# Optimization experiments

Hardware: AMD Instinct MI355X
Metric: run time of the kernel (lower is better)

Reference implementation:

```python
import jax, jax.numpy as jnp
import numpy as np

DIM = 1024
N_HEADS = 16
HEAD_DIM = DIM // N_HEADS


def setup_inputs() -> dict:
    key = jax.random.key(0)
    ks = jax.random.split(key, 5)
    B, L = 2, 2048
    q = jax.random.normal(ks[0], (B, L, DIM), dtype=jnp.float32)
    # nn.Linear weights: shape [out_features, in_features], applied as x @ W.T
    scale = 1.0 / np.sqrt(DIM)
    Wq = jax.random.normal(ks[1], (DIM, DIM), dtype=jnp.float32) * scale
    Wk = jax.random.normal(ks[2], (DIM, DIM), dtype=jnp.float32) * scale
    Wv = jax.random.normal(ks[3], (DIM, DIM), dtype=jnp.float32) * scale
    Wo = jax.random.normal(ks[4], (DIM, DIM), dtype=jnp.float32) * scale
    return {"q": q, "Wq": Wq, "Wk": Wk, "Wv": Wv, "Wo": Wo}


def reference(q, Wq, Wk, Wv, Wo):
    B, L, _ = q.shape
    kv = q  # self-attention (kv=None path)
    # projections: x @ W.T, then split heads: b l (h d) -> b h l d
    def split_heads(x):
        return x.reshape(B, L, N_HEADS, HEAD_DIM).transpose(0, 2, 1, 3)
    qh = split_heads(q @ Wq.T)
    kh = split_heads(kv @ Wk.T)
    vh = split_heads(kv @ Wv.T)
    # scaled dot-product attention; scale = sqrt(head_dim)
    scores = jnp.einsum('bhid,bhjd->bhij', qh, kh) / jnp.sqrt(
        jnp.asarray(HEAD_DIM, dtype=qh.dtype))
    attn = jax.nn.softmax(scores, axis=-1)
    out = jnp.einsum('bhij,bhjd->bhid', attn, vh)
    # b h l d -> b l (h d)
    out = out.transpose(0, 2, 1, 3).reshape(B, L, DIM)
    return out @ Wo.T
```

## Files before the change

### kernel.cpp

```cpp
#include <hip/hip_runtime.h>


#define DIMN 1024
#define NH 16
#define HD 64
#define BB 2
#define LL 2048

typedef float f32x4 __attribute__((ext_vector_type(4)));
typedef short s16x8 __attribute__((ext_vector_type(8)));

#define QSCALE 0.18033688011112042f

static __device__ __forceinline__ unsigned short f2bf(float f) {
  unsigned u = __float_as_uint(f);
  u += 0x7fffu + ((u >> 16) & 1u);
  return (unsigned short)(u >> 16);
}
static __device__ __forceinline__ unsigned packbf2(float lo, float hi) {
  return (unsigned)f2bf(lo) | ((unsigned)f2bf(hi) << 16);
}
static __device__ __forceinline__ float xexp2(float x) {
#if __has_builtin(__builtin_amdgcn_exp2f)
  return __builtin_amdgcn_exp2f(x);
#else
  return exp2f(x);
#endif
}
static __device__ __forceinline__ s16x8 cvt8(float4 a, float4 b) {
  s16x8 r;
  r[0] = (short)f2bf(a.x); r[1] = (short)f2bf(a.y);
  r[2] = (short)f2bf(a.z); r[3] = (short)f2bf(a.w);
  r[4] = (short)f2bf(b.x); r[5] = (short)f2bf(b.y);
  r[6] = (short)f2bf(b.z); r[7] = (short)f2bf(b.w);
  return r;
}
static __device__ __forceinline__ void gld16(const unsigned short* g,
                                             unsigned short* l) {
#if __has_builtin(__builtin_amdgcn_global_load_lds)
  __builtin_amdgcn_global_load_lds(
      (const __attribute__((address_space(1))) void*)g,
      (__attribute__((address_space(3))) void*)l, 16, 0, 0);
#else
  ((uint4*)l)[threadIdx.x & 63] = ((const uint4*)g)[0];
#endif
}

static __device__ __forceinline__ int vpos(int s128) {
  return (s128 & 0x60) | ((s128 & 0x0C) << 1) | ((s128 & 0x10) >> 2) | (s128 & 3);
}

__global__ __launch_bounds__(256) void cvt_all(
    const float* __restrict__ X, const float* __restrict__ Wq,
    const float* __restrict__ Wk, const float* __restrict__ Wv,
    const float* __restrict__ Wo, unsigned short* __restrict__ out) {
  const int blk = blockIdx.x;
  const float* src;
  unsigned short* dst;
  size_t off;
  if (blk < 2048) {
    src = X; dst = out; off = (size_t)blk * 2048;
  } else {
    int s = (blk - 2048) >> 9;
    src = (s == 0) ? Wq : (s == 1) ? Wk : (s == 2) ? Wv : Wo;
    dst = out + ((size_t)1 << 22) + (size_t)s * (1u << 20);
    off = (size_t)((blk - 2048) & 511) * 2048;
  }
  size_t i = off + (size_t)threadIdx.x * 8;
  float4 v0 = *(const float4*)(src + i);
  float4 v1 = *(const float4*)(src + i + 4);
  uint4 o;
  o.x = packbf2(v0.x, v0.y); o.y = packbf2(v0.z, v0.w);
  o.z = packbf2(v1.x, v1.y); o.w = packbf2(v1.z, v1.w);
  *(uint4*)(dst + i) = o;
}

__global__ __launch_bounds__(256) void gemm_qkv(
    const unsigned short* __restrict__ Xb, const unsigned short* __restrict__ Wb,
    unsigned short* __restrict__ Qb, unsigned short* __restrict__ Kb,
    unsigned short* __restrict__ VT) {
  __shared__ __align__(16) unsigned short Al[128 * 64];
  __shared__ __align__(16) unsigned short Bl[128 * 64];
  const int lin = blockIdx.x;
  const int xcd = lin & 7, sblk = lin >> 3;
  const int m0 = ((xcd & 3) * 8 + (sblk & 7)) * 128;
  const int n0g = ((xcd >> 2) * 12 + (sblk >> 3)) * 128;
  const int sel = n0g >> 10;
  const int tid = threadIdx.x;
  const int w = tid >> 6, lane = tid & 63;
  const int c = lane & 15, quad = lane >> 4;
  const int wm = (w & 1) * 64, wn = (w >> 1) * 64;

  f32x4 zero = {0.f, 0.f, 0.f, 0.f};
  f32x4 acc[4][4];
#pragma unroll
  for (int i = 0; i < 4; ++i)
#pragma unroll
    for (int j = 0; j < 4; ++j) acc[i][j] = zero;

  const int l8 = lane >> 3, p8 = lane & 7;
  const unsigned short* gA = Xb + (size_t)(m0 + w * 8 + l8) * DIMN + ((p8 ^ l8) * 8);
  const unsigned short* gB = Wb + (size_t)(n0g + w * 8 + l8) * DIMN + ((p8 ^ l8) * 8);
  unsigned short* lA = Al + (w * 8) * 64;
  unsigned short* lB = Bl + (w * 8) * 64;
  const int c7 = c & 7;

  for (int k0 = 0; k0 < DIMN; k0 += 64) {
    __syncthreads();
#pragma unroll
    for (int r = 0; r < 4; ++r) {
      gld16(gA + k0 + (size_t)(r * 32) * DIMN, lA + r * 32 * 64);
      gld16(gB + k0 + (size_t)(r * 32) * DIMN, lB + r * 32 * 64);
    }
    __syncthreads();
#pragma unroll
    for (int f = 0; f < 2; ++f) {
      const int rd = ((f * 4 + quad) ^ c7) * 8;
      s16x8 a[4], b[4];
#pragma unroll
      for (int i = 0; i < 4; ++i)
        a[i] = *(const s16x8*)&Al[(wm + i * 16 + c) * 64 + rd];
#pragma unroll
      for (int j = 0; j < 4; ++j)
        b[j] = *(const s16x8*)&Bl[(wn + j * 16 + c) * 64 + rd];
      if (sel != 2) {
#pragma unroll
        for (int i = 0; i < 4; ++i)
#pragma unroll
          for (int j = 0; j < 4; ++j)
            acc[i][j] = __builtin_amdgcn_mfma_f32_16x16x32_bf16(b[j], a[i], acc[i][j], 0, 0, 0);
      } else {
#pragma unroll
        for (int i = 0; i < 4; ++i)
#pragma unroll
          for (int j = 0; j < 4; ++j)
            acc[i][j] = __builtin_amdgcn_mfma_f32_16x16x32_bf16(a[i], b[j], acc[i][j], 0, 0, 0);
      }
    }
  }

  const int n0 = n0g & 1023;
  if (sel != 2) {
    unsigned short* Out = (sel == 0) ? Qb : Kb;
    const float scale = (sel == 0) ? QSCALE : 1.0f;
    const int bi = (m0 + wm) >> 11;
#pragma unroll
    for (int i = 0; i < 4; ++i) {
      const int li = (m0 + wm + i * 16 + c) & 2047;
#pragma unroll
      for (int j = 0; j < 4; ++j) {
        const int nq = n0 + wn + j * 16 + quad * 4;
        const int h = nq >> 6, d = nq & 63;
        uint2 st;
        st.x = packbf2(acc[i][j][0] * scale, acc[i][j][1] * scale);
        st.y = packbf2(acc[i][j][2] * scale, acc[i][j][3] * scale);
        *(uint2*)&Out[(((size_t)bi * NH + h) * LL + li) * HD + d] = st;
      }
    }
  } else {
    const int bi = m0 >> 11;
    const int mlo = m0 & 2047;
#pragma unroll
    for (int i = 0; i < 4; ++i) {
      const int pos = mlo + vpos(wm + i * 16 + quad * 4);
#pragma unroll
      for (int j = 0; j < 4; ++j) {
        const int nv = n0 + wn + j * 16 + c;
        const int h = nv >> 6, d = nv & 63;
        uint2 st;
        st.x = packbf2(acc[i][j][0], acc[i][j][1]);
        st.y = packbf2(acc[i][j][2], acc[i][j][3]);
        *(uint2*)&VT[(((size_t)bi * NH + h) * HD + d) * LL + pos] = st;
      }
    }
  }
}

__global__ __launch_bounds__(256) void gemm_o(
    const unsigned short* __restrict__ A, const unsigned short* __restrict__ Wob,
    float* __restrict__ Out) {
  __shared__ __align__(16) unsigned short Al[128 * 64];
  __shared__ __align__(16) unsigned short Bl[64 * 64];
  const int lin = blockIdx.x;
  const int xcd = lin & 7, sblk = lin >> 3;
  const int m0 = ((sblk >> 4) * 8 + xcd) * 128;
  const int n0 = (sblk & 15) * 64;
  const int tid = threadIdx.x;
  const int w = tid >> 6, lane = tid & 63;
  const int c = lane & 15, quad = lane >> 4;
  const int wm = (w & 1) * 64, wn = (w >> 1) * 32;

  f32x4 zero = {0.f, 0.f, 0.f, 0.f};
  f32x4 acc[4][2];
#pragma unroll
  for (int i = 0; i < 4; ++i)
#pragma unroll
    for (int j = 0; j < 2; ++j) acc[i][j] = zero;

  const int l8 = lane >> 3, p8 = lane & 7;
  const unsigned short* gA = A + (size_t)(m0 + w * 8 + l8) * DIMN + ((p8 ^ l8) * 8);
  const unsigned short* gB = Wob + (size_t)(n0 + w * 8 + l8) * DIMN + ((p8 ^ l8) * 8);
  unsigned short* lA = Al + (w * 8) * 64;
  unsigned short* lB = Bl + (w * 8) * 64;
  const int c7 = c & 7;

  for (int k0 = 0; k0 < DIMN; k0 += 64) {
    __syncthreads();
#pragma unroll
    for (int r = 0; r < 4; ++r)
      gld16(gA + k0 + (size_t)(r * 32) * DIMN, lA + r * 32 * 64);
#pragma unroll
    for (int r = 0; r < 2; ++r)
      gld16(gB + k0 + (size_t)(r * 32) * DIMN, lB + r * 32 * 64);
    __syncthreads();
#pragma unroll
    for (int f = 0; f < 2; ++f) {
      const int rd = ((f * 4 + quad) ^ c7) * 8;
      s16x8 a[4], b[2];
#pragma unroll
      for (int i = 0; i < 4; ++i)
        a[i] = *(const s16x8*)&Al[(wm + i * 16 + c) * 64 + rd];
#pragma unroll
      for (int j = 0; j < 2; ++j)
        b[j] = *(const s16x8*)&Bl[(wn + j * 16 + c) * 64 + rd];
#pragma unroll
      for (int i = 0; i < 4; ++i)
#pragma unroll
        for (int j = 0; j < 2; ++j)
          acc[i][j] = __builtin_amdgcn_mfma_f32_16x16x32_bf16(a[i], b[j], acc[i][j], 0, 0, 0);
    }
  }

#pragma unroll
  for (int i = 0; i < 4; ++i)
#pragma unroll
    for (int j = 0; j < 2; ++j)
#pragma unroll
      for (int r = 0; r < 4; ++r)
        Out[(size_t)(m0 + wm + i * 16 + quad * 4 + r) * DIMN + n0 + wn + j * 16 + c] =
            acc[i][j][r];
}

__global__ __launch_bounds__(256, 2) void attn7(
    const unsigned short* __restrict__ Qb, const unsigned short* __restrict__ Kb,
    const unsigned short* __restrict__ VT, unsigned short* __restrict__ AO) {
  __shared__ __align__(16) unsigned short Kl[2 * 128 * 64];
  __shared__ __align__(16) unsigned short Vtl[2 * 64 * 128];

  const int lin = blockIdx.x;
  const int xcd = lin & 7, sblk = lin >> 3;
  const int bh = (sblk >> 4) * 8 + xcd;
  const int qi = sblk & 15;
  const int tid = threadIdx.x;
  const int w = tid >> 6, lane = tid & 63;
  const int c = lane & 15, quad = lane >> 4;
  const int qa = qi * 128 + w * 16;
  const int qbr = qa + 64;

  const unsigned short* Qh = Qb + (size_t)bh * LL * HD;
  const unsigned short* Kh = Kb + (size_t)bh * LL * HD;
  const unsigned short* Vh = VT + (size_t)bh * HD * LL;

  s16x8 qA0 = *(const s16x8*)(Qh + (size_t)(qa + c) * HD + quad * 8);
  s16x8 qA1 = *(const s16x8*)(Qh + (size_t)(qa + c) * HD + 32 + quad * 8);
  s16x8 qB0 = *(const s16x8*)(Qh + (size_t)(qbr + c) * HD + quad * 8);
  s16x8 qB1 = *(const s16x8*)(Qh + (size_t)(qbr + c) * HD + 32 + quad * 8);

  f32x4 zero = {0.f, 0.f, 0.f, 0.f};
  f32x4 oA[4], oB[4];
  float lsumA = 0.f, lsumB = 0.f;
#pragma unroll
  for (int dc = 0; dc < 4; ++dc) { oA[dc] = zero; oB[dc] = zero; }

  const int l8 = lane >> 3, p8 = lane & 7;
  const unsigned short* gK = Kh + (size_t)(w * 32 + l8) * HD + ((p8 ^ l8) * 8);
  const int l16 = lane >> 4, p16 = lane & 15;
  const int vr0 = w * 16 + l16;
  const int vr1 = w * 16 + 4 + l16;
  const int vr2 = w * 16 + 8 + l16;
  const int vr3 = w * 16 + 12 + l16;
  const unsigned short* gV0 = Vh + (size_t)vr0 * LL + ((p16 ^ (vr0 & 15)) * 8);
  const unsigned short* gV1 = Vh + (size_t)vr1 * LL + ((p16 ^ (vr1 & 15)) * 8);
  const unsigned short* gV2 = Vh + (size_t)vr2 * LL + ((p16 ^ (vr2 & 15)) * 8);
  const unsigned short* gV3 = Vh + (size_t)vr3 * LL + ((p16 ^ (vr3 & 15)) * 8);

  const int kpa = (quad ^ (c & 7)) * 8;
  const int kpb = ((quad + 4) ^ (c & 7)) * 8;

#define STAGE(buf, k0)                                                        \
  do {                                                                        \
    unsigned short* lK_ = Kl + (buf) * (128 * 64) + (w * 32) * 64;            \
    unsigned short* lV_ = Vtl + (buf) * (64 * 128) + (w * 16) * 128;          \
    gld16(gK + (size_t)(k0) * HD, lK_);                                       \
    gld16(gK + (size_t)((k0) + 8) * HD, lK_ + 8 * 64);                        \
    gld16(gK + (size_t)((k0) + 16) * HD, lK_ + 16 * 64);                      \
    gld16(gK + (size_t)((k0) + 24) * HD, lK_ + 24 * 64);                      \
    gld16(gV0 + (k0), lV_);                                                   \
    gld16(gV1 + (k0), lV_ + 4 * 128);                                         \
    gld16(gV2 + (k0), lV_ + 8 * 128);                                         \
    gld16(gV3 + (k0), lV_ + 12 * 128);                                        \
  } while (0)

  STAGE(0, 0);

  for (int it = 0; it < LL / 128; ++it) {
    __syncthreads();
    if (it + 1 < LL / 128) STAGE((it + 1) & 1, (it + 1) * 128);
    const unsigned short* Kt = Kl + (it & 1) * (128 * 64);
    const unsigned short* Vt = Vtl + (it & 1) * (64 * 128);

#pragma unroll
    for (int g = 0; g < 2; ++g) {
      f32x4 sA[4], sB[4];
#pragma unroll
      for (int t4 = 0; t4 < 4; ++t4) {
        const unsigned short* kr = Kt + ((g * 4 + t4) * 16 + c) * 64;
        s16x8 kfa = *(const s16x8*)(kr + kpa);
        s16x8 kfb = *(const s16x8*)(kr + kpb);
        sA[t4] = __builtin_amdgcn_mfma_f32_16x16x32_bf16(kfa, qA0, zero, 0, 0, 0);
        sA[t4] = __builtin_amdgcn_mfma_f32_16x16x32_bf16(kfb, qA1, sA[t4], 0, 0, 0);
        sB[t4] = __builtin_amdgcn_mfma_f32_16x16x32_bf16(kfa, qB0, zero, 0, 0, 0);
        sB[t4] = __builtin_amdgcn_mfma_f32_16x16x32_bf16(kfb, qB1, sB[t4], 0, 0, 0);
      }
      float pA[4][4], pB[4][4];
      float accA = 0.f, accB = 0.f;
#pragma unroll
      for (int t4 = 0; t4 < 4; ++t4)
#pragma unroll
        for (int r = 0; r < 4; ++r) {
          float eA = xexp2(sA[t4][r]);
          float eB = xexp2(sB[t4][r]);
          pA[t4][r] = eA; accA += eA;
          pB[t4][r] = eB; accB += eB;
        }
      lsumA += accA;
      lsumB += accB;
#pragma unroll
      for (int kh = 0; kh < 2; ++kh) {
        const int kk = g * 2 + kh;
        unsigned puA[4], puB[4];
        puA[0] = __builtin_amdgcn_perm(__float_as_uint(pA[2 * kh][1]),
                                       __float_as_uint(pA[2 * kh][0]), 0x07060302u);
        puA[1] = __builtin_amdgcn_perm(__float_as_uint(pA[2 * kh][3]),
                                       __float_as_uint(pA[2 * kh][2]), 0x07060302u);
        puA[2] = __builtin_amdgcn_perm(__float_as_uint(pA[2 * kh + 1][1]),
                                       __float_as_uint(pA[2 * kh + 1][0]), 0x07060302u);
        puA[3] = __builtin_amdgcn_perm(__float_as_uint(pA[2 * kh + 1][3]),
                                       __float_as_uint(pA[2 * kh + 1][2]), 0x07060302u);
        puB[0] = __builtin_amdgcn_perm(__float_as_uint(pB[2 * kh][1]),
                                       __float_as_uint(pB[2 * kh][0]), 0x07060302u);
        puB[1] = __builtin_amdgcn_perm(__float_as_uint(pB[2 * kh][3]),
                                       __float_as_uint(pB[2 * kh][2]), 0x07060302u);
        puB[2] = __builtin_amdgcn_perm(__float_as_uint(pB[2 * kh + 1][1]),
                                       __float_as_uint(pB[2 * kh + 1][0]), 0x07060302u);
        puB[3] = __builtin_amdgcn_perm(__float_as_uint(pB[2 * kh + 1][3]),
                                       __float_as_uint(pB[2 * kh + 1][2]), 0x07060302u);
        s16x8 pfA = *(const s16x8*)puA;
        s16x8 pfB = *(const s16x8*)puB;
#pragma unroll
        for (int dc = 0; dc < 4; ++dc) {
          s16x8 vf = *(const s16x8*)(Vt + (dc * 16 + c) * 128 + (((kk * 4 + quad) ^ c) * 8));
          oA[dc] = __builtin_amdgcn_mfma_f32_16x16x32_bf16(vf, pfA, oA[dc], 0, 0, 0);
          oB[dc] = __builtin_amdgcn_mfma_f32_16x16x32_bf16(vf, pfB, oB[dc], 0, 0, 0);
        }
      }
    }
  }
#undef STAGE

  const int bi = bh >> 4, h = bh & 15;
  float lA = lsumA;
  lA += __shfl_xor(lA, 16);
  lA += __shfl_xor(lA, 32);
  float invA = 1.0f / lA;
  float lB = lsumB;
  lB += __shfl_xor(lB, 16);
  lB += __shfl_xor(lB, 32);
  float invB = 1.0f / lB;
  unsigned short* dstA = AO + ((size_t)bi * LL + qa + c) * DIMN + h * HD + quad * 4;
  unsigned short* dstB = AO + ((size_t)bi * LL + qbr + c) * DIMN + h * HD + quad * 4;
#pragma unroll
  for (int dc = 0; dc < 4; ++dc) {
    uint2 stA, stB;
    stA.x = packbf2(oA[dc][0] * invA, oA[dc][1] * invA);
    stA.y = packbf2(oA[dc][2] * invA, oA[dc][3] * invA);
    stB.x = packbf2(oB[dc][0] * invB, oB[dc][1] * invB);
    stB.y = packbf2(oB[dc][2] * invB, oB[dc][3] * invB);
    *(uint2*)(dstA + dc * 16) = stA;
    *(uint2*)(dstB + dc * 16) = stB;
  }
}

__global__ __launch_bounds__(64) void qkv_proj_f(
    const float* __restrict__ X, const float* __restrict__ Wq,
    const float* __restrict__ Wk, const float* __restrict__ Wv,
    unsigned short* __restrict__ Qb, unsigned short* __restrict__ Kb,
    unsigned short* __restrict__ VT) {
  const int m0 = blockIdx.x * 64;
  const int n0g = blockIdx.y * 64;
  const int sel = n0g >> 10;
  const int n0 = n0g & 1023;
  const float* W = (sel == 0) ? Wq : (sel == 1) ? Wk : Wv;
  const int lane = threadIdx.x;
  const int c = lane & 15, quad = lane >> 4;

  f32x4 zero = {0.f, 0.f, 0.f, 0.f};
  f32x4 acc[4][4];
#pragma unroll
  for (int i = 0; i < 4; ++i)
#pragma unroll
    for (int j = 0; j < 4; ++j) acc[i][j] = zero;

  const float* ab = X + (size_t)(m0 + c) * DIMN + quad * 8;
  const float* bb = W + (size_t)(n0 + c) * DIMN + quad * 8;

  for (int k0 = 0; k0 < DIMN; k0 += 32) {
    s16x8 a[4], b[4];
#pragma unroll
    for (int i = 0; i < 4; ++i) {
      const float* pp = ab + i * 16 * DIMN + k0;
      a[i] = cvt8(*(const float4*)pp, *(const float4*)(pp + 4));
    }
#pragma unroll
    for (int j = 0; j < 4; ++j) {
      const float* pp = bb + j * 16 * DIMN + k0;
      b[j] = cvt8(*(const float4*)pp, *(const float4*)(pp + 4));
    }
    if (sel != 2) {
#pragma unroll
      for (int i = 0; i < 4; ++i)
#pragma unroll
        for (int j = 0; j < 4; ++j)
          acc[i][j] = __builtin_amdgcn_mfma_f32_16x16x32_bf16(a[i], b[j], acc[i][j], 0, 0, 0);
    } else {
#pragma unroll
      for (int i = 0; i < 4; ++i)
#pragma unroll
        for (int j = 0; j < 4; ++j)
          acc[i][j] = __builtin_amdgcn_mfma_f32_16x16x32_bf16(b[j], a[i], acc[i][j], 0, 0, 0);
    }
  }

  if (sel != 2) {
    unsigned short* Out = (sel == 0) ? Qb : Kb;
    const float scale = (sel == 0) ? QSCALE : 1.0f;
#pragma unroll
    for (int i = 0; i < 4; ++i)
#pragma unroll
      for (int j = 0; j < 4; ++j)
#pragma unroll
        for (int r = 0; r < 4; ++r) {
          int row = m0 + i * 16 + quad * 4 + r;
          int nl = n0 + j * 16 + c;
          int bi = row >> 11, li = row & 2047;
          int h = nl >> 6, d = nl & 63;
          Out[(((size_t)bi * NH + h) * LL + li) * HD + d] = f2bf(acc[i][j][r] * scale);
        }
  } else {
#pragma unroll
    for (int i = 0; i < 4; ++i) {
#pragma unroll
      for (int j = 0; j < 4; ++j)
#pragma unroll
        for (int r = 0; r < 4; ++r) {
          int n = n0 + j * 16 + quad * 4 + r;
          int s128 = (m0 & 64) + i * 16 + c;
          int m = (m0 & ~127) + vpos(s128);
          int h = n >> 6, d = n & 63;
          int bi = m0 >> 11;
          VT[(((size_t)bi * NH + h) * HD + d) * LL + (m & 2047)] = f2bf(acc[i][j][r]);
        }
    }
  }
}

__global__ __launch_bounds__(64) void o_proj_f(
    const unsigned short* __restrict__ A, const float* __restrict__ Wo,
    float* __restrict__ Out) {
  const int m0 = blockIdx.x * 64, n0 = blockIdx.y * 64;
  const int lane = threadIdx.x;
  const int c = lane & 15, quad = lane >> 4;

  f32x4 zero = {0.f, 0.f, 0.f, 0.f};
  f32x4 acc[4][4];
#pragma unroll
  for (int i = 0; i < 4; ++i)
#pragma unroll
    for (int j = 0; j < 4; ++j) acc[i][j] = zero;

  const unsigned short* ab = A + (size_t)(m0 + c) * DIMN + quad * 8;
  const float* bb = Wo + (size_t)(n0 + c) * DIMN + quad * 8;

  for (int k0 = 0; k0 < DIMN; k0 += 32) {
    s16x8 a[4], b[4];
#pragma unroll
    for (int i = 0; i < 4; ++i) a[i] = *(const s16x8*)(ab + i * 16 * DIMN + k0);
#pragma unroll
    for (int j = 0; j < 4; ++j) {
      const float* pp = bb + j * 16 * DIMN + k0;
      b[j] = cvt8(*(const float4*)pp, *(const float4*)(pp + 4));
    }
#pragma unroll
    for (int i = 0; i < 4; ++i)
#pragma unroll
      for (int j = 0; j < 4; ++j)
        acc[i][j] = __builtin_amdgcn_mfma_f32_16x16x32_bf16(a[i], b[j], acc[i][j], 0, 0, 0);
  }

#pragma unroll
  for (int i = 0; i < 4; ++i)
#pragma unroll
    for (int j = 0; j < 4; ++j)
#pragma unroll
      for (int r = 0; r < 4; ++r)
        Out[(size_t)(m0 + i * 16 + quad * 4 + r) * DIMN + n0 + j * 16 + c] = acc[i][j][r];
}

extern "C" void kernel_launch(void* const* d_in, const int* in_sizes, int n_in,
                              void* d_out, int out_size, void* d_ws, size_t ws_size,
                              hipStream_t stream) {
  const float* X = (const float*)d_in[0];
  const float* Wq = (const float*)d_in[1];
  const float* Wk = (const float*)d_in[2];
  const float* Wv = (const float*)d_in[3];
  const float* Wo = (const float*)d_in[4];
  float* Out = (float*)d_out;

  const size_t M1 = (size_t)1 << 20;
  unsigned short* ws16 = (unsigned short*)d_ws;

  if (ws_size >= (size_t)48 * 1024 * 1024) {
    unsigned short* Xb = ws16;
    unsigned short* Wb = ws16 + 4 * M1;
    unsigned short* Qb = ws16 + 8 * M1;
    unsigned short* Kb = ws16 + 12 * M1;
    unsigned short* VT = ws16 + 16 * M1;
    unsigned short* AO = ws16 + 20 * M1;
    cvt_all<<<4096, 256, 0, stream>>>(X, Wq, Wk, Wv, Wo, ws16);
    gemm_qkv<<<768, 256, 0, stream>>>(Xb, Wb, Qb, Kb, VT);
    attn7<<<512, 256, 0, stream>>>(Qb, Kb, VT, AO);
    gemm_o<<<512, 256, 0, stream>>>(AO, Wb + 3 * M1, Out);
  } else {
    unsigned short* Qb = ws16;
    unsigned short* Kb = ws16 + 4 * M1;
    unsigned short* VT = ws16 + 8 * M1;
    unsigned short* AO = ws16 + 12 * M1;
    qkv_proj_f<<<dim3(64, 48), 64, 0, stream>>>(X, Wq, Wk, Wv, Qb, Kb, VT);
    attn7<<<512, 256, 0, stream>>>(Qb, Kb, VT, AO);
    o_proj_f<<<dim3(64, 16), 64, 0, stream>>>(AO, Wo, Out);
  }
}
```

Baseline: 174.2 us.

## Software-pipeline attention: overlap QK^T of next tile with PV of current

Restructures the attention main loop so QK^T and softmax for K tile it+1 run in the same iteration as the PV product for V tile it. This puts the exp/perm VALU work between MFMA bursts so the two can overlap. K and V staging are split so K is prefetched two tiles ahead and V one tile ahead. s_setprio raises wave priority around the MFMA phases. The cost is more live registers (probabilities for a whole tile are held across phases), which may cause spills at 2 waves per SIMD.

```diff
diff --git a/kernel.cpp b/kernel.cpp
--- a/kernel.cpp
+++ b/kernel.cpp
@@ -241,7 +241,7 @@
             acc[i][j][r];
 }
 
-__global__ __launch_bounds__(256, 2) void attn7(
+__global__ __launch_bounds__(256, 2) void attn8(
     const unsigned short* __restrict__ Qb, const unsigned short* __restrict__ Kb,
     const unsigned short* __restrict__ VT, unsigned short* __restrict__ AO) {
   __shared__ __align__(16) unsigned short Kl[2 * 128 * 64];
@@ -287,86 +287,137 @@
   const int kpa = (quad ^ (c & 7)) * 8;
   const int kpb = ((quad + 4) ^ (c & 7)) * 8;
 
-#define STAGE(buf, k0)                                                        \
+#define STAGE_K(buf, k0)                                                      \
   do {                                                                        \
     unsigned short* lK_ = Kl + (buf) * (128 * 64) + (w * 32) * 64;            \
-    unsigned short* lV_ = Vtl + (buf) * (64 * 128) + (w * 16) * 128;          \
     gld16(gK + (size_t)(k0) * HD, lK_);                                       \
     gld16(gK + (size_t)((k0) + 8) * HD, lK_ + 8 * 64);                        \
     gld16(gK + (size_t)((k0) + 16) * HD, lK_ + 16 * 64);                      \
     gld16(gK + (size_t)((k0) + 24) * HD, lK_ + 24 * 64);                      \
+  } while (0)
+#define STAGE_V(buf, k0)                                                      \
+  do {                                                                        \
+    unsigned short* lV_ = Vtl + (buf) * (64 * 128) + (w * 16) * 128;          \
     gld16(gV0 + (k0), lV_);                                                   \
     gld16(gV1 + (k0), lV_ + 4 * 128);                                         \
     gld16(gV2 + (k0), lV_ + 8 * 128);                                         \
     gld16(gV3 + (k0), lV_ + 12 * 128);                                        \
   } while (0)
 
-  STAGE(0, 0);
-
-  for (int it = 0; it < LL / 128; ++it) {
+#define QK_PHASE(Kt, g)                                                       \
+  do {                                                                        \
+    _Pragma("unroll")                                                         \
+    for (int t4 = 0; t4 < 4; ++t4) {                                          \
+      const unsigned short* kr = (Kt) + (((g) * 4 + t4) * 16 + c) * 64;       \
+      s16x8 kfa = *(const s16x8*)(kr + kpa);                                  \
+      s16x8 kfb = *(const s16x8*)(kr + kpb);                                  \
+      sA[t4] = __builtin_amdgcn_mfma_f32_16x16x32_bf16(kfa, qA0, zero, 0, 0, 0); \
+      sA[t4] = __builtin_amdgcn_mfma_f32_16x16x32_bf16(kfb, qA1, sA[t4], 0, 0, 0); \
+      sB[t4] = __builtin_amdgcn_mfma_f32_16x16x32_bf16(kfa, qB0, zero, 0, 0, 0); \
+      sB[t4] = __builtin_amdgcn_mfma_f32_16x16x32_bf16(kfb, qB1, sB[t4], 0, 0, 0); \
+    }                                                                         \
+  } while (0)
+
+#define SM_PHASE(g)                                                           \
+  do {                                                                        \
+    float pA[4][4], pB[4][4];                                                 \
+    float a0 = 0.f, a1 = 0.f, b0 = 0.f, b1 = 0.f;                             \
+    _Pragma("unroll")                                                         \
+    for (int t4 = 0; t4 < 4; ++t4)                                            \
+      _Pragma("unroll")                                                       \
+      for (int r = 0; r < 4; ++r) {                                           \
+        float eA = xexp2(sA[t4][r]);                                          \
+        float eB = xexp2(sB[t4][r]);                                          \
+        pA[t4][r] = eA; pB[t4][r] = eB;                                       \
+        if (t4 & 1) { a1 += eA; b1 += eB; } else { a0 += eA; b0 += eB; }      \
+      }                                                                       \
+    lsumA += a0 + a1; lsumB += b0 + b1;                                       \
+    _Pragma("unroll")                                                         \
+    for (int kh = 0; kh < 2; ++kh) {                                          \
+      unsigned puA[4], puB[4];                                                \
+      puA[0] = __builtin_amdgcn_perm(__float_as_uint(pA[2 * kh][1]),          \
+                                     __float_as_uint(pA[2 * kh][0]), 0x07060302u); \
+      puA[1] = __builtin_amdgcn_perm(__float_as_uint(pA[2 * kh][3]),          \
+                                     __float_as_uint(pA[2 * kh][2]), 0x07060302u); \
+      puA[2] = __builtin_amdgcn_perm(__float_as_uint(pA[2 * kh + 1][1]),      \
+                                     __float_as_uint(pA[2 * kh + 1][0]), 0x07060302u); \
+      puA[3] = __builtin_amdgcn_perm(__float_as_uint(pA[2 * kh + 1][3]),      \
+                                     __float_as_uint(pA[2 * kh + 1][2]), 0x07060302u); \
+      puB[0] = __builtin_amdgcn_perm(__float_as_uint(pB[2 * kh][1]),          \
+                                     __float_as_uint(pB[2 * kh][0]), 0x07060302u); \
+      puB[1] = __builtin_amdgcn_perm(__float_as_uint(pB[2 * kh][3]),          \
+                                     __float_as_uint(pB[2 * kh][2]), 0x07060302u); \
+      puB[2] = __builtin_amdgcn_perm(__float_as_uint(pB[2 * kh + 1][1]),      \
+                                     __float_as_uint(pB[2 * kh + 1][0]), 0x07060302u); \
+      puB[3] = __builtin_amdgcn_perm(__float_as_uint(pB[2 * kh + 1][3]),      \
+                                     __float_as_uint(pB[2 * kh + 1][2]), 0x07060302u); \
+      pfA[(g) * 2 + kh] = *(const s16x8*)puA;                                 \
+      pfB[(g) * 2 + kh] = *(const s16x8*)puB;                                 \
+    }                                                                         \
+  } while (0)
+
+#define PV_PHASE(Vt, kk0)                                                     \
+  do {                                                                        \
+    _Pragma("unroll")                                                         \
+    for (int kh = 0; kh < 2; ++kh) {                                          \
+      const int kk = (kk0) + kh;                                              \
+      _Pragma("unroll")                                                       \
+      for (int dc = 0; dc < 4; ++dc) {                                        \
+        s16x8 vf = *(const s16x8*)((Vt) + (dc * 16 + c) * 128 +               \
+                                   (((kk * 4 + quad) ^ c) * 8));              \
+        oA[dc] = __builtin_amdgcn_mfma_f32_16x16x32_bf16(vf, pfA[kk], oA[dc], 0, 0, 0); \
+        oB[dc] = __builtin_amdgcn_mfma_f32_16x16x32_bf16(vf, pfB[kk], oB[dc], 0, 0, 0); \
+      }                                                                       \
+    }                                                                         \
+  } while (0)
+
+  s16x8 pfA[4], pfB[4];
+  f32x4 sA[4], sB[4];
+
+  STAGE_K(0, 0);
+  STAGE_V(0, 0);
+  STAGE_K(1, 128);
+  __syncthreads();
+  {
+    const unsigned short* Kt = Kl;
+    QK_PHASE(Kt, 0);
+    SM_PHASE(0);
+    QK_PHASE(Kt, 1);
+    SM_PHASE(1);
+  }
+
+  for (int it = 0; it < LL / 128 - 1; ++it) {
     __syncthreads();
-    if (it + 1 < LL / 128) STAGE((it + 1) & 1, (it + 1) * 128);
-    const unsigned short* Kt = Kl + (it & 1) * (128 * 64);
+    STAGE_V((it + 1) & 1, (it + 1) * 128);
+    if (it + 2 < LL / 128) STAGE_K(it & 1, (it + 2) * 128);
+    const unsigned short* Kt = Kl + ((it + 1) & 1) * (128 * 64);
     const unsigned short* Vt = Vtl + (it & 1) * (64 * 128);
 
-#pragma unroll
-    for (int g = 0; g < 2; ++g) {
-      f32x4 sA[4], sB[4];
-#pragma unroll
-      for (int t4 = 0; t4 < 4; ++t4) {
-        const unsigned short* kr = Kt + ((g * 4 + t4) * 16 + c) * 64;
-        s16x8 kfa = *(const s16x8*)(kr + kpa);
-        s16x8 kfb = *(const s16x8*)(kr + kpb);
-        sA[t4] = __builtin_amdgcn_mfma_f32_16x16x32_bf16(kfa, qA0, zero, 0, 0, 0);
-        sA[t4] = __builtin_amdgcn_mfma_f32_16x16x32_bf16(kfb, qA1, sA[t4], 0, 0, 0);
-        sB[t4] = __builtin_amdgcn_mfma_f32_16x16x32_bf16(kfa, qB0, zero, 0, 0, 0);
-        sB[t4] = __builtin_amdgcn_mfma_f32_16x16x32_bf16(kfb, qB1, sB[t4], 0, 0, 0);
-      }
-      float pA[4][4], pB[4][4];
-      float accA = 0.f, accB = 0.f;
-#pragma unroll
-      for (int t4 = 0; t4 < 4; ++t4)
-#pragma unroll
-        for (int r = 0; r < 4; ++r) {
-          float eA = xexp2(sA[t4][r]);
-          float eB = xexp2(sB[t4][r]);
-          pA[t4][r] = eA; accA += eA;
-          pB[t4][r] = eB; accB += eB;
-        }
-      lsumA += accA;
-      lsumB += accB;
-#pragma unroll
-      for (int kh = 0; kh < 2; ++kh) {
-        const int kk = g * 2 + kh;
-        unsigned puA[4], puB[4];
-        puA[0] = __builtin_amdgcn_perm(__float_as_uint(pA[2 * kh][1]),
-                                       __float_as_uint(pA[2 * kh][0]), 0x07060302u);
-        puA[1] = __builtin_amdgcn_perm(__float_as_uint(pA[2 * kh][3]),
-                                       __float_as_uint(pA[2 * kh][2]), 0x07060302u);
-        puA[2] = __builtin_amdgcn_perm(__float_as_uint(pA[2 * kh + 1][1]),
-                                       __float_as_uint(pA[2 * kh + 1][0]), 0x07060302u);
-        puA[3] = __builtin_amdgcn_perm(__float_as_uint(pA[2 * kh + 1][3]),
-                                       __float_as_uint(pA[2 * kh + 1][2]), 0x07060302u);
-        puB[0] = __builtin_amdgcn_perm(__float_as_uint(pB[2 * kh][1]),
-                                       __float_as_uint(pB[2 * kh][0]), 0x07060302u);
-        puB[1] = __builtin_amdgcn_perm(__float_as_uint(pB[2 * kh][3]),
-                                       __float_as_uint(pB[2 * kh][2]), 0x07060302u);
-        puB[2] = __builtin_amdgcn_perm(__float_as_uint(pB[2 * kh + 1][1]),
-                                       __float_as_uint(pB[2 * kh + 1][0]), 0x07060302u);
-        puB[3] = __builtin_amdgcn_perm(__float_as_uint(pB[2 * kh + 1][3]),
-                                       __float_as_uint(pB[2 * kh + 1][2]), 0x07060302u);
-        s16x8 pfA = *(const s16x8*)puA;
-        s16x8 pfB = *(const s16x8*)puB;
-#pragma unroll
-        for (int dc = 0; dc < 4; ++dc) {
-          s16x8 vf = *(const s16x8*)(Vt + (dc * 16 + c) * 128 + (((kk * 4 + quad) ^ c) * 8));
-          oA[dc] = __builtin_amdgcn_mfma_f32_16x16x32_bf16(vf, pfA, oA[dc], 0, 0, 0);
-          oB[dc] = __builtin_amdgcn_mfma_f32_16x16x32_bf16(vf, pfB, oB[dc], 0, 0, 0);
-        }
-      }
-    }
-  }
-#undef STAGE
+    __builtin_amdgcn_s_setprio(1);
+    QK_PHASE(Kt, 0);
+    PV_PHASE(Vt, 0);
+    __builtin_amdgcn_s_setprio(0);
+    SM_PHASE(0);
+    __builtin_amdgcn_s_setprio(1);
+    QK_PHASE(Kt, 1);
+    PV_PHASE(Vt, 2);
+    __builtin_amdgcn_s_setprio(0);
+    SM_PHASE(1);
+  }
+
+  __syncthreads();
+  {
+    const unsigned short* Vt = Vtl + ((LL / 128 - 1) & 1) * (64 * 128);
+    __builtin_amdgcn_s_setprio(1);
+    PV_PHASE(Vt, 0);
+    PV_PHASE(Vt, 2);
+    __builtin_amdgcn_s_setprio(0);
+  }
+#undef STAGE_K
+#undef STAGE_V
+#undef QK_PHASE
+#undef SM_PHASE
+#undef PV_PHASE
 
   const int bi = bh >> 4, h = bh & 15;
   float lA = lsumA;
@@ -538,7 +589,7 @@
     unsigned short* AO = ws16 + 20 * M1;
     cvt_all<<<4096, 256, 0, stream>>>(X, Wq, Wk, Wv, Wo, ws16);
     gemm_qkv<<<768, 256, 0, stream>>>(Xb, Wb, Qb, Kb, VT);
-    attn7<<<512, 256, 0, stream>>>(Qb, Kb, VT, AO);
+    attn8<<<512, 256, 0, stream>>>(Qb, Kb, VT, AO);
     gemm_o<<<512, 256, 0, stream>>>(AO, Wb + 3 * M1, Out);
   } else {
     unsigned short* Qb = ws16;
@@ -546,7 +597,7 @@
     unsigned short* VT = ws16 + 8 * M1;
     unsigned short* AO = ws16 + 12 * M1;
     qkv_proj_f<<<dim3(64, 48), 64, 0, stream>>>(X, Wq, Wk, Wv, Qb, Kb, VT);
-    attn7<<<512, 256, 0, stream>>>(Qb, Kb, VT, AO);
+    attn8<<<512, 256, 0, stream>>>(Qb, Kb, VT, AO);
     o_proj_f<<<dim3(64, 16), 64, 0, stream>>>(AO, Wo, Out);
   }
 }
```

After: 178.2 us. +2.3%, slower.

## Split attention KV range across two wave groups per block and reduce via LDS

Applied to the files above, without the earlier changes.

The attention kernel now runs 512 threads per block. Two groups of four waves each process half of the 2048-key sequence for the same 128 queries, using 64-key tiles with their own double-buffered LDS staging. At the end, the second group writes its partial outputs and row sums to LDS, and the first group combines them, normalises and stores. This doubles the waves per block to hide latency and raise occupancy, at the cost of an extra LDS reduction and more barriers per tile. It relies on the existing max-free softmax (no running max), which is what makes the partial sums simply additive.

```diff
diff --git a/kernel.cpp b/kernel.cpp
--- a/kernel.cpp
+++ b/kernel.cpp
@@ -241,11 +241,11 @@
             acc[i][j][r];
 }
 
-__global__ __launch_bounds__(256, 2) void attn7(
+__global__ __launch_bounds__(512, 4) void attn9(
     const unsigned short* __restrict__ Qb, const unsigned short* __restrict__ Kb,
     const unsigned short* __restrict__ VT, unsigned short* __restrict__ AO) {
-  __shared__ __align__(16) unsigned short Kl[2 * 128 * 64];
-  __shared__ __align__(16) unsigned short Vtl[2 * 64 * 128];
+  __shared__ __align__(16) unsigned short Kl[2][2][64 * 64];
+  __shared__ __align__(16) unsigned short Vtl[2][2][64 * 64];
 
   const int lin = blockIdx.x;
   const int xcd = lin & 7, sblk = lin >> 3;
@@ -253,13 +253,14 @@
   const int qi = sblk & 15;
   const int tid = threadIdx.x;
   const int w = tid >> 6, lane = tid & 63;
+  const int half = w >> 2, wl = w & 3;
   const int c = lane & 15, quad = lane >> 4;
-  const int qa = qi * 128 + w * 16;
+  const int qa = qi * 128 + wl * 16;
   const int qbr = qa + 64;
 
   const unsigned short* Qh = Qb + (size_t)bh * LL * HD;
-  const unsigned short* Kh = Kb + (size_t)bh * LL * HD;
-  const unsigned short* Vh = VT + (size_t)bh * HD * LL;
+  const unsigned short* Kh = Kb + (size_t)bh * LL * HD + (size_t)half * 1024 * HD;
+  const unsigned short* Vh = VT + (size_t)bh * HD * LL + half * 1024;
 
   s16x8 qA0 = *(const s16x8*)(Qh + (size_t)(qa + c) * HD + quad * 8);
   s16x8 qA1 = *(const s16x8*)(Qh + (size_t)(qa + c) * HD + 32 + quad * 8);
@@ -273,121 +274,135 @@
   for (int dc = 0; dc < 4; ++dc) { oA[dc] = zero; oB[dc] = zero; }
 
   const int l8 = lane >> 3, p8 = lane & 7;
-  const unsigned short* gK = Kh + (size_t)(w * 32 + l8) * HD + ((p8 ^ l8) * 8);
-  const int l16 = lane >> 4, p16 = lane & 15;
-  const int vr0 = w * 16 + l16;
-  const int vr1 = w * 16 + 4 + l16;
-  const int vr2 = w * 16 + 8 + l16;
-  const int vr3 = w * 16 + 12 + l16;
-  const unsigned short* gV0 = Vh + (size_t)vr0 * LL + ((p16 ^ (vr0 & 15)) * 8);
-  const unsigned short* gV1 = Vh + (size_t)vr1 * LL + ((p16 ^ (vr1 & 15)) * 8);
-  const unsigned short* gV2 = Vh + (size_t)vr2 * LL + ((p16 ^ (vr2 & 15)) * 8);
-  const unsigned short* gV3 = Vh + (size_t)vr3 * LL + ((p16 ^ (vr3 & 15)) * 8);
-
-  const int kpa = (quad ^ (c & 7)) * 8;
-  const int kpb = ((quad + 4) ^ (c & 7)) * 8;
-
-#define STAGE(buf, k0)                                                        \
+  const unsigned short* gK = Kh + (size_t)(wl * 16 + l8) * HD + ((p8 ^ l8) * 8);
+  const int vr = wl * 16 + l8;
+  const unsigned short* gV = Vh + (size_t)vr * LL + ((p8 ^ l8) * 8);
+
+  const int c7 = c & 7;
+  const int kpa = (quad ^ c7) * 8;
+  const int kpb = ((quad + 4) ^ c7) * 8;
+
+#define STAGE(buf, kv)                                                        \
   do {                                                                        \
-    unsigned short* lK_ = Kl + (buf) * (128 * 64) + (w * 32) * 64;            \
-    unsigned short* lV_ = Vtl + (buf) * (64 * 128) + (w * 16) * 128;          \
-    gld16(gK + (size_t)(k0) * HD, lK_);                                       \
-    gld16(gK + (size_t)((k0) + 8) * HD, lK_ + 8 * 64);                        \
-    gld16(gK + (size_t)((k0) + 16) * HD, lK_ + 16 * 64);                      \
-    gld16(gK + (size_t)((k0) + 24) * HD, lK_ + 24 * 64);                      \
-    gld16(gV0 + (k0), lV_);                                                   \
-    gld16(gV1 + (k0), lV_ + 4 * 128);                                         \
-    gld16(gV2 + (k0), lV_ + 8 * 128);                                         \
-    gld16(gV3 + (k0), lV_ + 12 * 128);                                        \
+    unsigned short* lK_ = &Kl[half][buf][(wl * 16) * 64];                     \
+    unsigned short* lV_ = &Vtl[half][buf][(wl * 16) * 64];                    \
+    gld16(gK + (size_t)(kv) * HD, lK_);                                       \
+    gld16(gK + (size_t)((kv) + 8) * HD, lK_ + 8 * 64);                        \
+    gld16(gV + (kv), lV_);                                                    \
+    gld16(gV + (size_t)8 * LL + (kv), lV_ + 8 * 64);                          \
   } while (0)
 
   STAGE(0, 0);
 
-  for (int it = 0; it < LL / 128; ++it) {
+  for (int it = 0; it < 16; ++it) {
     __syncthreads();
-    if (it + 1 < LL / 128) STAGE((it + 1) & 1, (it + 1) * 128);
-    const unsigned short* Kt = Kl + (it & 1) * (128 * 64);
-    const unsigned short* Vt = Vtl + (it & 1) * (64 * 128);
-
-#pragma unroll
-    for (int g = 0; g < 2; ++g) {
-      f32x4 sA[4], sB[4];
-#pragma unroll
-      for (int t4 = 0; t4 < 4; ++t4) {
-        const unsigned short* kr = Kt + ((g * 4 + t4) * 16 + c) * 64;
-        s16x8 kfa = *(const s16x8*)(kr + kpa);
-        s16x8 kfb = *(const s16x8*)(kr + kpb);
-        sA[t4] = __builtin_amdgcn_mfma_f32_16x16x32_bf16(kfa, qA0, zero, 0, 0, 0);
-        sA[t4] = __builtin_amdgcn_mfma_f32_16x16x32_bf16(kfb, qA1, sA[t4], 0, 0, 0);
-        sB[t4] = __builtin_amdgcn_mfma_f32_16x16x32_bf16(kfa, qB0, zero, 0, 0, 0);
-        sB[t4] = __builtin_amdgcn_mfma_f32_16x16x32_bf16(kfb, qB1, sB[t4], 0, 0, 0);
+    if (it + 1 < 16) STAGE((it + 1) & 1, (it + 1) * 64);
+    const unsigned short* Kt = &Kl[half][it & 1][0];
+    const unsigned short* Vt = &Vtl[half][it & 1][0];
+
+    f32x4 sA[4], sB[4];
+#pragma unroll
+    for (int t4 = 0; t4 < 4; ++t4) {
+      const unsigned short* kr = Kt + (t4 * 16 + c) * 64;
+      s16x8 kfa = *(const s16x8*)(kr + kpa);
+      s16x8 kfb = *(const s16x8*)(kr + kpb);
+      sA[t4] = __builtin_amdgcn_mfma_f32_16x16x32_bf16(kfa, qA0, zero, 0, 0, 0);
+      sA[t4] = __builtin_amdgcn_mfma_f32_16x16x32_bf16(kfb, qA1, sA[t4], 0, 0, 0);
+      sB[t4] = __builtin_amdgcn_mfma_f32_16x16x32_bf16(kfa, qB0, zero, 0, 0, 0);
+      sB[t4] = __builtin_amdgcn_mfma_f32_16x16x32_bf16(kfb, qB1, sB[t4], 0, 0, 0);
+    }
+
+    float pA[4][4], pB[4][4];
+    float a0 = 0.f, a1 = 0.f, b0 = 0.f, b1 = 0.f;
+#pragma unroll
+    for (int t4 = 0; t4 < 4; ++t4)
+#pragma unroll
+      for (int r = 0; r < 4; ++r) {
+        float eA = xexp2(sA[t4][r]);
+        float eB = xexp2(sB[t4][r]);
+        pA[t4][r] = eA; pB[t4][r] = eB;
+        if (t4 & 1) { a1 += eA; b1 += eB; } else { a0 += eA; b0 += eB; }
       }
-      float pA[4][4], pB[4][4];
-      float accA = 0.f, accB = 0.f;
-#pragma unroll
-      for (int t4 = 0; t4 < 4; ++t4)
-#pragma unroll
-        for (int r = 0; r < 4; ++r) {
-          float eA = xexp2(sA[t4][r]);
-          float eB = xexp2(sB[t4][r]);
-          pA[t4][r] = eA; accA += eA;
-          pB[t4][r] = eB; accB += eB;
-        }
-      lsumA += accA;
-      lsumB += accB;
-#pragma unroll
-      for (int kh = 0; kh < 2; ++kh) {
-        const int kk = g * 2 + kh;
-        unsigned puA[4], puB[4];
-        puA[0] = __builtin_amdgcn_perm(__float_as_uint(pA[2 * kh][1]),
-                                       __float_as_uint(pA[2 * kh][0]), 0x07060302u);
-        puA[1] = __builtin_amdgcn_perm(__float_as_uint(pA[2 * kh][3]),
-                                       __float_as_uint(pA[2 * kh][2]), 0x07060302u);
-        puA[2] = __builtin_amdgcn_perm(__float_as_uint(pA[2 * kh + 1][1]),
-                                       __float_as_uint(pA[2 * kh + 1][0]), 0x07060302u);
-        puA[3] = __builtin_amdgcn_perm(__float_as_uint(pA[2 * kh + 1][3]),
-                                       __float_as_uint(pA[2 * kh + 1][2]), 0x07060302u);
-        puB[0] = __builtin_amdgcn_perm(__float_as_uint(pB[2 * kh][1]),
-                                       __float_as_uint(pB[2 * kh][0]), 0x07060302u);
-        puB[1] = __builtin_amdgcn_perm(__float_as_uint(pB[2 * kh][3]),
-                                       __float_as_uint(pB[2 * kh][2]), 0x07060302u);
-        puB[2] = __builtin_amdgcn_perm(__float_as_uint(pB[2 * kh + 1][1]),
-                                       __float_as_uint(pB[2 * kh + 1][0]), 0x07060302u);
-        puB[3] = __builtin_amdgcn_perm(__float_as_uint(pB[2 * kh + 1][3]),
-                                       __float_as_uint(pB[2 * kh + 1][2]), 0x07060302u);
-        s16x8 pfA = *(const s16x8*)puA;
-        s16x8 pfB = *(const s16x8*)puB;
-#pragma unroll
-        for (int dc = 0; dc < 4; ++dc) {
-          s16x8 vf = *(const s16x8*)(Vt + (dc * 16 + c) * 128 + (((kk * 4 + quad) ^ c) * 8));
-          oA[dc] = __builtin_amdgcn_mfma_f32_16x16x32_bf16(vf, pfA, oA[dc], 0, 0, 0);
-          oB[dc] = __builtin_amdgcn_mfma_f32_16x16x32_bf16(vf, pfB, oB[dc], 0, 0, 0);
-        }
+    lsumA += a0 + a1; lsumB += b0 + b1;
+
+    s16x8 pfA[2], pfB[2];
+#pragma unroll
+    for (int kh = 0; kh < 2; ++kh) {
+      unsigned puA[4], puB[4];
+      puA[0] = __builtin_amdgcn_perm(__float_as_uint(pA[2 * kh][1]),
+                                     __float_as_uint(pA[2 * kh][0]), 0x07060302u);
+      puA[1] = __builtin_amdgcn_perm(__float_as_uint(pA[2 * kh][3]),
+                                     __float_as_uint(pA[2 * kh][2]), 0x07060302u);
+      puA[2] = __builtin_amdgcn_perm(__float_as_uint(pA[2 * kh + 1][1]),
+                                     __float_as_uint(pA[2 * kh + 1][0]), 0x07060302u);
+      puA[3] = __builtin_amdgcn_perm(__float_as_uint(pA[2 * kh + 1][3]),
+                                     __float_as_uint(pA[2 * kh + 1][2]), 0x07060302u);
+      puB[0] = __builtin_amdgcn_perm(__float_as_uint(pB[2 * kh][1]),
+                                     __float_as_uint(pB[2 * kh][0]), 0x07060302u);
+      puB[1] = __builtin_amdgcn_perm(__float_as_uint(pB[2 * kh][3]),
+                                     __float_as_uint(pB[2 * kh][2]), 0x07060302u);
+      puB[2] = __builtin_amdgcn_perm(__float_as_uint(pB[2 * kh + 1][1]),
+                                     __float_as_uint(pB[2 * kh + 1][0]), 0x07060302u);
+      puB[3] = __builtin_amdgcn_perm(__float_as_uint(pB[2 * kh + 1][3]),
+                                     __float_as_uint(pB[2 * kh + 1][2]), 0x07060302u);
+      pfA[kh] = *(const s16x8*)puA;
+      pfB[kh] = *(const s16x8*)puB;
+    }
+
+#pragma unroll
+    for (int kh = 0; kh < 2; ++kh) {
+#pragma unroll
+      for (int dc = 0; dc < 4; ++dc) {
+        s16x8 vf = *(const s16x8*)(Vt + (dc * 16 + c) * 64 +
+                                   (((kh * 4 + quad) ^ c7) * 8));
+        oA[dc] = __builtin_amdgcn_mfma_f32_16x16x32_bf16(vf, pfA[kh], oA[dc], 0, 0, 0);
+        oB[dc] = __builtin_amdgcn_mfma_f32_16x16x32_bf16(vf, pfB[kh], oB[dc], 0, 0, 0);
       }
     }
   }
 #undef STAGE
 
-  const int bi = bh >> 4, h = bh & 15;
   float lA = lsumA;
   lA += __shfl_xor(lA, 16);
   lA += __shfl_xor(lA, 32);
-  float invA = 1.0f / lA;
   float lB = lsumB;
   lB += __shfl_xor(lB, 16);
   lB += __shfl_xor(lB, 32);
-  float invB = 1.0f / lB;
-  unsigned short* dstA = AO + ((size_t)bi * LL + qa + c) * DIMN + h * HD + quad * 4;
-  unsigned short* dstB = AO + ((size_t)bi * LL + qbr + c) * DIMN + h * HD + quad * 4;
-#pragma unroll
-  for (int dc = 0; dc < 4; ++dc) {
-    uint2 stA, stB;
-    stA.x = packbf2(oA[dc][0] * invA, oA[dc][1] * invA);
-    stA.y = packbf2(oA[dc][2] * invA, oA[dc][3] * invA);
-    stB.x = packbf2(oB[dc][0] * invB, oB[dc][1] * invB);
-    stB.y = packbf2(oB[dc][2] * invB, oB[dc][3] * invB);
-    *(uint2*)(dstA + dc * 16) = stA;
-    *(uint2*)(dstB + dc * 16) = stB;
+
+  f32x4* ob4 = (f32x4*)&Kl[0][0][0];
+  float* lb = (float*)&Vtl[0][0][0];
+
+  __syncthreads();
+  if (half == 1) {
+#pragma unroll
+    for (int dc = 0; dc < 4; ++dc) {
+      ob4[((wl * 2 + 0) * 4 + dc) * 64 + lane] = oA[dc];
+      ob4[((wl * 2 + 1) * 4 + dc) * 64 + lane] = oB[dc];
+    }
+    lb[(wl * 2 + 0) * 64 + lane] = lA;
+    lb[(wl * 2 + 1) * 64 + lane] = lB;
+  }
+  __syncthreads();
+  if (half == 0) {
+    lA += lb[(wl * 2 + 0) * 64 + lane];
+    lB += lb[(wl * 2 + 1) * 64 + lane];
+    float invA = 1.0f / lA;
+    float invB = 1.0f / lB;
+    const int bi = bh >> 4, h = bh & 15;
+    unsigned short* dstA = AO + ((size_t)bi * LL + qa + c) * DIMN + h * HD + quad * 4;
+    unsigned short* dstB = AO + ((size_t)bi * LL + qbr + c) * DIMN + h * HD + quad * 4;
+#pragma unroll
+    for (int dc = 0; dc < 4; ++dc) {
+      f32x4 sa = oA[dc] + ob4[((wl * 2 + 0) * 4 + dc) * 64 + lane];
+      f32x4 sb = oB[dc] + ob4[((wl * 2 + 1) * 4 + dc) * 64 + lane];
+      uint2 stA, stB;
+      stA.x = packbf2(sa[0] * invA, sa[1] * invA);
+      stA.y = packbf2(sa[2] * invA, sa[3] * invA);
+      stB.x = packbf2(sb[0] * invB, sb[1] * invB);
+      stB.y = packbf2(sb[2] * invB, sb[3] * invB);
+      *(uint2*)(dstA + dc * 16) = stA;
+      *(uint2*)(dstB + dc * 16) = stB;
+    }
   }
 }
 
@@ -538,7 +553,7 @@
     unsigned short* AO = ws16 + 20 * M1;
     cvt_all<<<4096, 256, 0, stream>>>(X, Wq, Wk, Wv, Wo, ws16);
     gemm_qkv<<<768, 256, 0, stream>>>(Xb, Wb, Qb, Kb, VT);
-    attn7<<<512, 256, 0, stream>>>(Qb, Kb, VT, AO);
+    attn9<<<512, 512, 0, stream>>>(Qb, Kb, VT, AO);
     gemm_o<<<512, 256, 0, stream>>>(AO, Wb + 3 * M1, Out);
   } else {
     unsigned short* Qb = ws16;
@@ -546,7 +561,7 @@
     unsigned short* VT = ws16 + 8 * M1;
     unsigned short* AO = ws16 + 12 * M1;
     qkv_proj_f<<<dim3(64, 48), 64, 0, stream>>>(X, Wq, Wk, Wv, Qb, Kb, VT);
-    attn7<<<512, 256, 0, stream>>>(Qb, Kb, VT, AO);
+    attn9<<<512, 512, 0, stream>>>(Qb, Kb, VT, AO);
     o_proj_f<<<dim3(64, 16), 64, 0, stream>>>(AO, Wo, Out);
   }
 }
```

Measured after the change: 176.4 us. About the same (+1.2%).
